# Optimization experiments

Hardware: AMD Instinct MI355X
Metric: run time of the kernel (lower is better)

Reference implementation:

```python
import jax, jax.numpy as jnp
import numpy as np

B, T, I, H = 512, 1024, 50, 32  # batch, seq_len, input_size, hidden_size


def setup_inputs() -> dict:
    key = jax.random.key(0)
    ks = jax.random.split(key, 13)
    s = 1.0 / np.sqrt(H)  # PyTorch LSTM/Linear uniform init bound

    def u(k, shape):
        return jax.random.uniform(k, shape, jnp.float32, -s, s)

    return {
        "x": jax.random.normal(ks[0], (B, T, I), jnp.float32),
        # forward direction LSTM params (gate order: i, f, g, o)
        "w_ih_f": u(ks[1], (4 * H, I)),
        "w_hh_f": u(ks[2], (4 * H, H)),
        "b_ih_f": u(ks[3], (4 * H,)),
        "b_hh_f": u(ks[4], (4 * H,)),
        # reverse direction LSTM params
        "w_ih_r": u(ks[5], (4 * H, I)),
        "w_hh_r": u(ks[6], (4 * H, H)),
        "b_ih_r": u(ks[7], (4 * H,)),
        "b_hh_r": u(ks[8], (4 * H,)),
        # FC head
        "fc1_w": u(ks[9], (2 * H, 2 * H)),
        "fc1_b": u(ks[10], (2 * H,)),
        "fc3_w": u(ks[11], (1, 2 * H)),
        "fc3_b": u(ks[12], (1,)),
    }


def _lstm_scan(x_proj, w_hh):
    # x_proj: (T, B, 4H) = precomputed input projections + biases
    b = x_proj.shape[1]
    h0 = jnp.zeros((b, H), x_proj.dtype)
    c0 = jnp.zeros((b, H), x_proj.dtype)

    def step(carry, xp):
        h, c = carry
        z = xp + h @ w_hh.T  # (B, 4H)
        i, f, g, o = jnp.split(z, 4, axis=-1)
        c = jax.nn.sigmoid(f) * c + jax.nn.sigmoid(i) * jnp.tanh(g)
        h = jax.nn.sigmoid(o) * jnp.tanh(c)
        return (h, c), h

    _, hs = jax.lax.scan(step, (h0, c0), x_proj)
    return hs  # (T, B, H)


def reference(x, w_ih_f, w_hh_f, b_ih_f, b_hh_f,
              w_ih_r, w_hh_r, b_ih_r, b_hh_r,
              fc1_w, fc1_b, fc3_w, fc3_b):
    xt = jnp.swapaxes(x, 0, 1)  # (T, B, I) time-major for scan
    # batch all input projections up front (big GEMM instead of per-step)
    pf = xt @ w_ih_f.T + (b_ih_f + b_hh_f)          # (T, B, 4H)
    pr = xt[::-1] @ w_ih_r.T + (b_ih_r + b_hh_r)    # reversed time

    hf = _lstm_scan(pf, w_hh_f)           # (T, B, H)
    hr = _lstm_scan(pr, w_hh_r)[::-1]     # flip back to forward time order

    out = jnp.concatenate([hf, hr], axis=-1)  # (T, B, 2H)
    out = jnp.swapaxes(out, 0, 1)             # (B, T, 2H)
    out = out @ fc1_w.T + fc1_b               # fc1
    # dropout(p=0.2) is identity in eval/inference mode
    out = out @ fc3_w.T + fc3_b               # fc3 -> (B, T, 1)
    return out
```

## Files before the change

### kernel.cpp

```cpp
#include <hip/hip_runtime.h>

#define BB 512
#define TT 1024
#define II 50
#define HH 32
#define CH 16
#define NCH (TT / CH)
#define RSLOT 32

typedef float v2f __attribute__((ext_vector_type(2)));
typedef float v4f __attribute__((ext_vector_type(4)));
typedef short v8s __attribute__((ext_vector_type(8)));

__device__ __forceinline__ float fast_rcp(float x) { return __builtin_amdgcn_rcpf(x); }
__device__ __forceinline__ float sigm(float x) { return fast_rcp(1.f + __expf(-x)); }
__device__ __forceinline__ float tanh_(float x) {
    return 1.f - 2.f * fast_rcp(1.f + __expf(2.f * x));
}
__device__ __forceinline__ float hadd(v2f v) { return v.x + v.y; }
__device__ __forceinline__ short bf16rne(float f) {
    unsigned u = __float_as_uint(f);
    u += 0x7FFF + ((u >> 16) & 1);
    return (short)(u >> 16);
}

__global__ void init_out_kernel(float* __restrict__ out,
                                const float* __restrict__ fc1_b,
                                const float* __restrict__ fc3_w,
                                const float* __restrict__ fc3_b,
                                int n) {
    int idx = blockIdx.x * blockDim.x + threadIdx.x;
    float b = fc3_b[0];
    #pragma unroll
    for (int k = 0; k < 64; ++k) b += fc3_w[k] * fc1_b[k];
    if (idx < n) out[idx] = b;
}

__global__ void __launch_bounds__(128, 1) lstm_pc_kernel(
    const float* __restrict__ x,
    const float* __restrict__ w_ih_f, const float* __restrict__ w_hh_f,
    const float* __restrict__ b_ih_f, const float* __restrict__ b_hh_f,
    const float* __restrict__ w_ih_r, const float* __restrict__ w_hh_r,
    const float* __restrict__ b_ih_r, const float* __restrict__ b_hh_r,
    const float* __restrict__ fc1_w, const float* __restrict__ fc3_w,
    float* __restrict__ out)
{
    __shared__ float ringF[RSLOT * 256];
    __shared__ float hbuf[2][HH][65];
    __shared__ __align__(16) float hst[64];

    const int tid  = threadIdx.x;
    const int lane = tid & 63;
    const int wave = tid >> 6;
    const int b    = blockIdx.x;
    float* outb = out + (size_t)b * TT;

    if (wave == 1) {
        const float* xb = x + (size_t)b * TT * II;
        const int nl = lane & 15;
        const int q  = lane >> 4;
        const float* wih[2] = {w_ih_f, w_ih_r};

        v8s Bf[2][8][2];
        #pragma unroll
        for (int d = 0; d < 2; ++d)
            #pragma unroll
            for (int nt = 0; nt < 8; ++nt) {
                const int n = nt * 16 + nl;
                #pragma unroll
                for (int kf = 0; kf < 2; ++kf)
                    #pragma unroll
                    for (int j = 0; j < 8; ++j) {
                        const int k = kf * 32 + q * 8 + j;
                        Bf[d][nt][kf][j] = (k < II) ? bf16rne(wih[d][n * II + k])
                                                    : (short)0;
                    }
            }

        auto cidx = [](int g) -> int {
            return (g < 32) ? 2 * g
                 : (g < 64) ? 2 * (g - 32) + 1
                 : (g < 96) ? 64 + 2 * (g - 64)
                            : 64 + 2 * (g - 96) + 1;
        };

        auto produce_chunk = [&](int c) {
            #pragma unroll
            for (int d = 0; d < 2; ++d) {
                const int S = c * CH + nl;
                const int t = d ? (TT - 1 - S) : S;
                const float* xr = xb + (size_t)t * II;
                v8s A0, A1;
                #pragma unroll
                for (int j = 0; j < 8; ++j) A0[j] = bf16rne(xr[q * 8 + j]);
                #pragma unroll
                for (int j = 0; j < 8; ++j) {
                    const int k = 32 + q * 8 + j;
                    A1[j] = (k < II) ? bf16rne(xr[k]) : (short)0;
                }
                #pragma unroll
                for (int nt = 0; nt < 8; ++nt) {
                    v4f acc = {0.f, 0.f, 0.f, 0.f};
                    acc = __builtin_amdgcn_mfma_f32_16x16x32_bf16(A0, Bf[d][nt][0], acc, 0, 0, 0);
                    acc = __builtin_amdgcn_mfma_f32_16x16x32_bf16(A1, Bf[d][nt][1], acc, 0, 0, 0);
                    const int col = d * 128 + cidx(nt * 16 + nl);
                    #pragma unroll
                    for (int r = 0; r < 4; ++r) {
                        const int slot = (c * CH + q * 4 + r) & (RSLOT - 1);
                        ringF[slot * 256 + col] = acc[r];
                    }
                }
            }
        };
        auto flush = [&](int m) {
            if (lane < 32) {
                const int d   = lane >> 4;
                const int idx = lane & 15;
                const int ti  = m * CH + idx;
                const int col = ti & 63;
                float d0 = 0.f, d1 = 0.f, d2 = 0.f, d3 = 0.f;
                #pragma unroll
                for (int k = 0; k < HH; k += 4) {
                    d0 += hbuf[d][k    ][col];
                    d1 += hbuf[d][k + 1][col];
                    d2 += hbuf[d][k + 2][col];
                    d3 += hbuf[d][k + 3][col];
                }
                const int t = d ? (TT - 1 - ti) : ti;
                atomicAdd(&outb[t], (d0 + d1) + (d2 + d3));
            }
        };

        produce_chunk(0);
        __syncthreads();
        for (int n = 0; n < NCH; ++n) {
            if (n + 1 < NCH) produce_chunk(n + 1);
            if (n >= 1) flush(n - 1);
            __syncthreads();
        }
        flush(NCH - 1);
    } else {
        const int d = lane >> 5;
        const int k = lane & 31;
        const float* w_hh = d ? w_hh_r : w_hh_f;
        const float* bi   = d ? b_ih_r : b_ih_f;
        const float* bh   = d ? b_hh_r : b_hh_f;

        v2f wp[4][16];
        float bb[4];
        #pragma unroll
        for (int D = 0; D < 4; ++D) {
            const int row = D * 32 + k;
            #pragma unroll
            for (int j = 0; j < 16; ++j) {
                wp[D][j].x = w_hh[row * HH + 2 * j];
                wp[D][j].y = w_hh[row * HH + 2 * j + 1];
            }
            bb[D] = bi[row] + bh[row];
        }

        float wc = 0.f;
        {
            const int j = d * HH + k;
            #pragma unroll
            for (int n = 0; n < 64; ++n) wc += fc3_w[n] * fc1_w[n * 64 + j];
        }

        hst[lane] = 0.f;
        float c = 0.f;

        __syncthreads();

        for (int n = 0; n < NCH; ++n) {
            const int slot0 = (n & 1) * CH;
            const int col0  = (n & 3) * CH;
            #pragma unroll
            for (int u = 0; u < CH; ++u) {
                const float* rp = &ringF[(slot0 + u) * 256 + d * 128 + 2 * k];
                const v2f xz1 = *(const v2f*)rp;
                const v2f xz2 = *(const v2f*)(rp + 64);

                float4 h4[8];
                #pragma unroll
                for (int j = 0; j < 8; ++j)
                    h4[j] = *(const float4*)&hst[d * 32 + 4 * j];

                v2f aA[4], aB[4];
                #pragma unroll
                for (int D = 0; D < 4; ++D) {
                    aA[D] = (v2f){bb[D], 0.f};
                    aB[D] = (v2f){0.f, 0.f};
                }
                #pragma unroll
                for (int j = 0; j < 8; ++j) {
                    v2f p0 = {h4[j].x, h4[j].y};
                    v2f p1 = {h4[j].z, h4[j].w};
                    #pragma unroll
                    for (int D = 0; D < 4; ++D) {
                        aA[D] = __builtin_elementwise_fma(p0, wp[D][2 * j    ], aA[D]);
                        aB[D] = __builtin_elementwise_fma(p1, wp[D][2 * j + 1], aB[D]);
                    }
                }
                const float zi = xz1.x + hadd(aA[0] + aB[0]);
                const float zf = xz1.y + hadd(aA[1] + aB[1]);
                const float zg = xz2.x + hadd(aA[2] + aB[2]);
                const float zo = xz2.y + hadd(aA[3] + aB[3]);

                const float gi = sigm(zi);
                const float gf = sigm(zf);
                const float gg = tanh_(zg);
                const float go = sigm(zo);

                c = fmaf(gf, c, gi * gg);
                const float h = go * tanh_(c);

                hst[lane] = h;
                hbuf[d][k][col0 + u] = h * wc;
                asm volatile("" ::: "memory");
            }
            __syncthreads();
        }
    }
}

extern "C" void kernel_launch(void* const* d_in, const int* in_sizes, int n_in,
                              void* d_out, int out_size, void* d_ws, size_t ws_size,
                              hipStream_t stream) {
    const float* x      = (const float*)d_in[0];
    const float* w_ih_f = (const float*)d_in[1];
    const float* w_hh_f = (const float*)d_in[2];
    const float* b_ih_f = (const float*)d_in[3];
    const float* b_hh_f = (const float*)d_in[4];
    const float* w_ih_r = (const float*)d_in[5];
    const float* w_hh_r = (const float*)d_in[6];
    const float* b_ih_r = (const float*)d_in[7];
    const float* b_hh_r = (const float*)d_in[8];
    const float* fc1_w  = (const float*)d_in[9];
    const float* fc1_b  = (const float*)d_in[10];
    const float* fc3_w  = (const float*)d_in[11];
    const float* fc3_b  = (const float*)d_in[12];
    float* out = (float*)d_out;

    const int n = BB * TT;
    init_out_kernel<<<(n + 255) / 256, 256, 0, stream>>>(out, fc1_b, fc3_w, fc3_b, n);

    lstm_pc_kernel<<<BB, 128, 0, stream>>>(
        x, w_ih_f, w_hh_f, b_ih_f, b_hh_f,
        w_ih_r, w_hh_r, b_ih_r, b_hh_r,
        fc1_w, fc3_w, out);
}
```

Before: 428.9 us.

## Use fp16 dot2 for recurrent matvec and prefetch chunk input projections

The recurrent h·W_hh product now stores the hidden state and weights as fp16 pairs and uses the v_dot2 f32-accumulate instruction. This halves the LDS reads of h per step and roughly halves the FMA instruction count on the serial critical path. The input projections for a whole chunk are also loaded into registers before the step loop. The cost is lower precision in h and W_hh, which may drift over 1024 recurrent steps, and higher register pressure.

```diff
diff --git a/kernel.cpp b/kernel.cpp
--- a/kernel.cpp
+++ b/kernel.cpp
@@ -11,18 +11,19 @@
 typedef float v2f __attribute__((ext_vector_type(2)));
 typedef float v4f __attribute__((ext_vector_type(4)));
 typedef short v8s __attribute__((ext_vector_type(8)));
+typedef _Float16 v2h __attribute__((ext_vector_type(2)));
 
 __device__ __forceinline__ float fast_rcp(float x) { return __builtin_amdgcn_rcpf(x); }
 __device__ __forceinline__ float sigm(float x) { return fast_rcp(1.f + __expf(-x)); }
 __device__ __forceinline__ float tanh_(float x) {
     return 1.f - 2.f * fast_rcp(1.f + __expf(2.f * x));
 }
-__device__ __forceinline__ float hadd(v2f v) { return v.x + v.y; }
 __device__ __forceinline__ short bf16rne(float f) {
     unsigned u = __float_as_uint(f);
     u += 0x7FFF + ((u >> 16) & 1);
     return (short)(u >> 16);
 }
+__device__ __forceinline__ v2h asv2h(int v) { return __builtin_bit_cast(v2h, v); }
 
 __global__ void init_out_kernel(float* __restrict__ out,
                                 const float* __restrict__ fc1_b,
@@ -47,7 +48,7 @@
 {
     __shared__ float ringF[RSLOT * 256];
     __shared__ float hbuf[2][HH][65];
-    __shared__ __align__(16) float hst[64];
+    __shared__ __align__(16) _Float16 hsth[64];
 
     const int tid  = threadIdx.x;
     const int lane = tid & 63;
@@ -146,15 +147,15 @@
         const float* bi   = d ? b_ih_r : b_ih_f;
         const float* bh   = d ? b_hh_r : b_hh_f;
 
-        v2f wp[4][16];
+        v2h wph[4][16];
         float bb[4];
         #pragma unroll
         for (int D = 0; D < 4; ++D) {
             const int row = D * 32 + k;
             #pragma unroll
             for (int j = 0; j < 16; ++j) {
-                wp[D][j].x = w_hh[row * HH + 2 * j];
-                wp[D][j].y = w_hh[row * HH + 2 * j + 1];
+                wph[D][j].x = (_Float16)w_hh[row * HH + 2 * j];
+                wph[D][j].y = (_Float16)w_hh[row * HH + 2 * j + 1];
             }
             bb[D] = bi[row] + bh[row];
         }
@@ -166,7 +167,7 @@
             for (int n = 0; n < 64; ++n) wc += fc3_w[n] * fc1_w[n * 64 + j];
         }
 
-        hst[lane] = 0.f;
+        hsth[lane] = (_Float16)0.f;
         float c = 0.f;
 
         __syncthreads();
@@ -174,37 +175,48 @@
         for (int n = 0; n < NCH; ++n) {
             const int slot0 = (n & 1) * CH;
             const int col0  = (n & 3) * CH;
+
+            v2f xz1b[CH], xz2b[CH];
             #pragma unroll
             for (int u = 0; u < CH; ++u) {
                 const float* rp = &ringF[(slot0 + u) * 256 + d * 128 + 2 * k];
-                const v2f xz1 = *(const v2f*)rp;
-                const v2f xz2 = *(const v2f*)(rp + 64);
-
-                float4 h4[8];
-                #pragma unroll
-                for (int j = 0; j < 8; ++j)
-                    h4[j] = *(const float4*)&hst[d * 32 + 4 * j];
-
-                v2f aA[4], aB[4];
+                xz1b[u] = *(const v2f*)rp;
+                xz2b[u] = *(const v2f*)(rp + 64);
+            }
+
+            #pragma unroll
+            for (int u = 0; u < CH; ++u) {
+                int4 hw0 = *(const int4*)&hsth[d * 32];
+                int4 hw1 = *(const int4*)&hsth[d * 32 + 8];
+                int4 hw2 = *(const int4*)&hsth[d * 32 + 16];
+                int4 hw3 = *(const int4*)&hsth[d * 32 + 24];
+
+                float zA[4], zB[4];
+                #pragma unroll
+                for (int D = 0; D < 4; ++D) { zA[D] = bb[D]; zB[D] = 0.f; }
                 #pragma unroll
                 for (int D = 0; D < 4; ++D) {
-                    aA[D] = (v2f){bb[D], 0.f};
-                    aB[D] = (v2f){0.f, 0.f};
-                }
-                #pragma unroll
-                for (int j = 0; j < 8; ++j) {
-                    v2f p0 = {h4[j].x, h4[j].y};
-                    v2f p1 = {h4[j].z, h4[j].w};
-                    #pragma unroll
-                    for (int D = 0; D < 4; ++D) {
-                        aA[D] = __builtin_elementwise_fma(p0, wp[D][2 * j    ], aA[D]);
-                        aB[D] = __builtin_elementwise_fma(p1, wp[D][2 * j + 1], aB[D]);
-                    }
-                }
-                const float zi = xz1.x + hadd(aA[0] + aB[0]);
-                const float zf = xz1.y + hadd(aA[1] + aB[1]);
-                const float zg = xz2.x + hadd(aA[2] + aB[2]);
-                const float zo = xz2.y + hadd(aA[3] + aB[3]);
+                    zA[D] = __builtin_amdgcn_fdot2(asv2h(hw0.x), wph[D][0],  zA[D], false);
+                    zB[D] = __builtin_amdgcn_fdot2(asv2h(hw0.y), wph[D][1],  zB[D], false);
+                    zA[D] = __builtin_amdgcn_fdot2(asv2h(hw0.z), wph[D][2],  zA[D], false);
+                    zB[D] = __builtin_amdgcn_fdot2(asv2h(hw0.w), wph[D][3],  zB[D], false);
+                    zA[D] = __builtin_amdgcn_fdot2(asv2h(hw1.x), wph[D][4],  zA[D], false);
+                    zB[D] = __builtin_amdgcn_fdot2(asv2h(hw1.y), wph[D][5],  zB[D], false);
+                    zA[D] = __builtin_amdgcn_fdot2(asv2h(hw1.z), wph[D][6],  zA[D], false);
+                    zB[D] = __builtin_amdgcn_fdot2(asv2h(hw1.w), wph[D][7],  zB[D], false);
+                    zA[D] = __builtin_amdgcn_fdot2(asv2h(hw2.x), wph[D][8],  zA[D], false);
+                    zB[D] = __builtin_amdgcn_fdot2(asv2h(hw2.y), wph[D][9],  zB[D], false);
+                    zA[D] = __builtin_amdgcn_fdot2(asv2h(hw2.z), wph[D][10], zA[D], false);
+                    zB[D] = __builtin_amdgcn_fdot2(asv2h(hw2.w), wph[D][11], zB[D], false);
+                    zA[D] = __builtin_amdgcn_fdot2(asv2h(hw3.x), wph[D][12], zA[D], false);
+                    zB[D] = __builtin_amdgcn_fdot2(asv2h(hw3.y), wph[D][13], zB[D], false);
+                    zA[D] = __builtin_amdgcn_fdot2(asv2h(hw3.z), wph[D][14], zA[D], false);
+                    zB[D] = __builtin_amdgcn_fdot2(asv2h(hw3.w), wph[D][15], zB[D], false);
+                }
+                const float zi = xz1b[u].x + (zA[0] + zB[0]);
+                const float zf = xz1b[u].y + (zA[1] + zB[1]);
+                const float zg = xz2b[u].x + (zA[2] + zB[2]);
+                const float zo = xz2b[u].y + (zA[3] + zB[3]);
 
                 const float gi = sigm(zi);
                 const float gf = sigm(zf);
@@ -214,7 +226,7 @@
                 c = fmaf(gf, c, gi * gg);
                 const float h = go * tanh_(c);
 
-                hst[lane] = h;
+                hsth[lane] = (_Float16)h;
                 hbuf[d][k][col0 + u] = h * wc;
                 asm volatile("" ::: "memory");
             }
```

Result: no change. 431.4 us (+0.6%).

## Process two batch rows per block with fp16 dot2 recurrence and fp16 ring

Applied to the files above, without the earlier changes.

Each block now handles two batch sequences, so the recurrent wave interleaves two independent LSTM chains to hide latency. The recurrent matvec switches from fp32 FMAs to packed fp16 fdot2 with fp16 weights and hidden state, and input projections are stored in LDS as fp16 to fit both sequences. Grid is halved to 256 blocks. This trades precision in h, W_hh and the projections for fewer instructions and better ILP on the serial critical path, but reduces the number of blocks available to fill the GPU.

```diff
diff --git a/kernel.cpp b/kernel.cpp
--- a/kernel.cpp
+++ b/kernel.cpp
@@ -11,18 +11,19 @@
 typedef float v2f __attribute__((ext_vector_type(2)));
 typedef float v4f __attribute__((ext_vector_type(4)));
 typedef short v8s __attribute__((ext_vector_type(8)));
+typedef _Float16 v2h __attribute__((ext_vector_type(2)));
 
 __device__ __forceinline__ float fast_rcp(float x) { return __builtin_amdgcn_rcpf(x); }
 __device__ __forceinline__ float sigm(float x) { return fast_rcp(1.f + __expf(-x)); }
 __device__ __forceinline__ float tanh_(float x) {
     return 1.f - 2.f * fast_rcp(1.f + __expf(2.f * x));
 }
-__device__ __forceinline__ float hadd(v2f v) { return v.x + v.y; }
 __device__ __forceinline__ short bf16rne(float f) {
     unsigned u = __float_as_uint(f);
     u += 0x7FFF + ((u >> 16) & 1);
     return (short)(u >> 16);
 }
+__device__ __forceinline__ v2h asv2h(int v) { return __builtin_bit_cast(v2h, v); }
 
 __global__ void init_out_kernel(float* __restrict__ out,
                                 const float* __restrict__ fc1_b,
@@ -45,18 +46,20 @@
     const float* __restrict__ fc1_w, const float* __restrict__ fc3_w,
     float* __restrict__ out)
 {
-    __shared__ float ringF[RSLOT * 256];
-    __shared__ float hbuf[2][HH][65];
-    __shared__ __align__(16) float hst[64];
+    __shared__ _Float16 ringH[RSLOT * 512];
+    __shared__ float hbuf[2][2][HH][33];
+    __shared__ __align__(16) _Float16 hsth[2][64];
 
     const int tid  = threadIdx.x;
     const int lane = tid & 63;
     const int wave = tid >> 6;
-    const int b    = blockIdx.x;
-    float* outb = out + (size_t)b * TT;
+    const int bp   = blockIdx.x;
+    const float* xb[2]  = {x + (size_t)(2 * bp) * TT * II,
+                           x + (size_t)(2 * bp + 1) * TT * II};
+    float* outp[2] = {out + (size_t)(2 * bp) * TT,
+                      out + (size_t)(2 * bp + 1) * TT};
 
     if (wave == 1) {
-        const float* xb = x + (size_t)b * TT * II;
         const int nl = lane & 15;
         const int q  = lane >> 4;
         const float* wih[2] = {w_ih_f, w_ih_r};
@@ -86,49 +89,50 @@
 
         auto produce_chunk = [&](int c) {
             #pragma unroll
-            for (int d = 0; d < 2; ++d) {
-                const int S = c * CH + nl;
-                const int t = d ? (TT - 1 - S) : S;
-                const float* xr = xb + (size_t)t * II;
-                v8s A0, A1;
+            for (int bb = 0; bb < 2; ++bb)
                 #pragma unroll
-                for (int j = 0; j < 8; ++j) A0[j] = bf16rne(xr[q * 8 + j]);
-                #pragma unroll
-                for (int j = 0; j < 8; ++j) {
-                    const int k = 32 + q * 8 + j;
-                    A1[j] = (k < II) ? bf16rne(xr[k]) : (short)0;
+                for (int d = 0; d < 2; ++d) {
+                    const int S = c * CH + nl;
+                    const int t = d ? (TT - 1 - S) : S;
+                    const float* xr = xb[bb] + (size_t)t * II;
+                    v8s A0, A1;
+                    #pragma unroll
+                    for (int j = 0; j < 8; ++j) A0[j] = bf16rne(xr[q * 8 + j]);
+                    #pragma unroll
+                    for (int j = 0; j < 8; ++j) {
+                        const int k = 32 + q * 8 + j;
+                        A1[j] = (k < II) ? bf16rne(xr[k]) : (short)0;
+                    }
+                    #pragma unroll
+                    for (int nt = 0; nt < 8; ++nt) {
+                        v4f acc = {0.f, 0.f, 0.f, 0.f};
+                        acc = __builtin_amdgcn_mfma_f32_16x16x32_bf16(A0, Bf[d][nt][0], acc, 0, 0, 0);
+                        acc = __builtin_amdgcn_mfma_f32_16x16x32_bf16(A1, Bf[d][nt][1], acc, 0, 0, 0);
+                        const int col = bb * 256 + d * 128 + cidx(nt * 16 + nl);
+                        #pragma unroll
+                        for (int r = 0; r < 4; ++r) {
+                            const int slot = (c * CH + q * 4 + r) & (RSLOT - 1);
+                            ringH[slot * 512 + col] = (_Float16)acc[r];
+                        }
+                    }
                 }
-                #pragma unroll
-                for (int nt = 0; nt < 8; ++nt) {
-                    v4f acc = {0.f, 0.f, 0.f, 0.f};
-                    acc = __builtin_amdgcn_mfma_f32_16x16x32_bf16(A0, Bf[d][nt][0], acc, 0, 0, 0);
-                    acc = __builtin_amdgcn_mfma_f32_16x16x32_bf16(A1, Bf[d][nt][1], acc, 0, 0, 0);
-                    const int col = d * 128 + cidx(nt * 16 + nl);
-                    #pragma unroll
-                    for (int r = 0; r < 4; ++r) {
-                        const int slot = (c * CH + q * 4 + r) & (RSLOT - 1);
-                        ringF[slot * 256 + col] = acc[r];
-                    }
-                }
-            }
         };
         auto flush = [&](int m) {
-            if (lane < 32) {
-                const int d   = lane >> 4;
-                const int idx = lane & 15;
-                const int ti  = m * CH + idx;
-                const int col = ti & 63;
-                float d0 = 0.f, d1 = 0.f, d2 = 0.f, d3 = 0.f;
-                #pragma unroll
-                for (int k = 0; k < HH; k += 4) {
-                    d0 += hbuf[d][k    ][col];
-                    d1 += hbuf[d][k + 1][col];
-                    d2 += hbuf[d][k + 2][col];
-                    d3 += hbuf[d][k + 3][col];
-                }
-                const int t = d ? (TT - 1 - ti) : ti;
-                atomicAdd(&outb[t], (d0 + d1) + (d2 + d3));
+            const int bb  = lane >> 5;
+            const int dd  = (lane >> 4) & 1;
+            const int idx = lane & 15;
+            const int ti  = m * CH + idx;
+            const int col = ti & 31;
+            float d0 = 0.f, d1 = 0.f, d2 = 0.f, d3 = 0.f;
+            #pragma unroll
+            for (int k = 0; k < HH; k += 4) {
+                d0 += hbuf[bb][dd][k    ][col];
+                d1 += hbuf[bb][dd][k + 1][col];
+                d2 += hbuf[bb][dd][k + 2][col];
+                d3 += hbuf[bb][dd][k + 3][col];
             }
+            const int t = dd ? (TT - 1 - ti) : ti;
+            atomicAdd(&outp[bb][t], (d0 + d1) + (d2 + d3));
         };
 
         produce_chunk(0);
@@ -146,17 +150,17 @@
         const float* bi   = d ? b_ih_r : b_ih_f;
         const float* bh   = d ? b_hh_r : b_hh_f;
 
-        v2f wp[4][16];
-        float bb[4];
+        v2h wph[4][16];
+        float bias4[4];
         #pragma unroll
         for (int D = 0; D < 4; ++D) {
             const int row = D * 32 + k;
             #pragma unroll
             for (int j = 0; j < 16; ++j) {
-                wp[D][j].x = w_hh[row * HH + 2 * j];
-                wp[D][j].y = w_hh[row * HH + 2 * j + 1];
+                wph[D][j].x = (_Float16)w_hh[row * HH + 2 * j];
+                wph[D][j].y = (_Float16)w_hh[row * HH + 2 * j + 1];
             }
-            bb[D] = bi[row] + bh[row];
+            bias4[D] = bi[row] + bh[row];
         }
 
         float wc = 0.f;
@@ -166,57 +170,106 @@
             for (int n = 0; n < 64; ++n) wc += fc3_w[n] * fc1_w[n * 64 + j];
         }
 
-        hst[lane] = 0.f;
-        float c = 0.f;
+        hsth[0][lane] = (_Float16)0.f;
+        hsth[1][lane] = (_Float16)0.f;
+        float cA = 0.f, cB = 0.f;
 
         __syncthreads();
 
         for (int n = 0; n < NCH; ++n) {
             const int slot0 = (n & 1) * CH;
-            const int col0  = (n & 3) * CH;
-            #pragma unroll
-            for (int u = 0; u < CH; ++u) {
-                const float* rp = &ringF[(slot0 + u) * 256 + d * 128 + 2 * k];
-                const v2f xz1 = *(const v2f*)rp;
-                const v2f xz2 = *(const v2f*)(rp + 64);
-
-                float4 h4[8];
+            const int col0  = (n & 1) * CH;
+            #pragma unroll
+            for (int half = 0; half < 2; ++half) {
+                int pA1[8], pA2[8], pB1[8], pB2[8];
                 #pragma unroll
-                for (int j = 0; j < 8; ++j)
-                    h4[j] = *(const float4*)&hst[d * 32 + 4 * j];
-
-                v2f aA[4], aB[4];
-                #pragma unroll
-                for (int D = 0; D < 4; ++D) {
-                    aA[D] = (v2f){bb[D], 0.f};
-                    aB[D] = (v2f){0.f, 0.f};
+                for (int u = 0; u < 8; ++u) {
+                    const int base = (slot0 + half * 8 + u) * 512 + d * 128 + 2 * k;
+                    pA1[u] = *(const int*)&ringH[base];
+                    pA2[u] = *(const int*)&ringH[base + 64];
+                    pB1[u] = *(const int*)&ringH[base + 256];
+                    pB2[u] = *(const int*)&ringH[base + 256 + 64];
                 }
                 #pragma unroll
-                for (int j = 0; j < 8; ++j) {
-                    v2f p0 = {h4[j].x, h4[j].y};
-                    v2f p1 = {h4[j].z, h4[j].w};
+                for (int u = 0; u < 8; ++u) {
+                    int4 aw0 = *(const int4*)&hsth[0][d * 32];
+                    int4 aw1 = *(const int4*)&hsth[0][d * 32 + 8];
+                    int4 aw2 = *(const int4*)&hsth[0][d * 32 + 16];
+                    int4 aw3 = *(const int4*)&hsth[0][d * 32 + 24];
+                    int4 bw0 = *(const int4*)&hsth[1][d * 32];
+                    int4 bw1 = *(const int4*)&hsth[1][d * 32 + 8];
+                    int4 bw2 = *(const int4*)&hsth[1][d * 32 + 16];
+                    int4 bw3 = *(const int4*)&hsth[1][d * 32 + 24];
+
+                    float zAa[4], zBa[4], zAb[4], zBb[4];
                     #pragma unroll
                     for (int D = 0; D < 4; ++D) {
-                        aA[D] = __builtin_elementwise_fma(p0, wp[D][2 * j    ], aA[D]);
-                        aB[D] = __builtin_elementwise_fma(p1, wp[D][2 * j + 1], aB[D]);
-                    }
+                        zAa[D] = bias4[D]; zBa[D] = 0.f;
+                        zAb[D] = bias4[D]; zBb[D] = 0.f;
+                    }
+                    #pragma unroll
+                    for (int D = 0; D < 4; ++D) {
+                        zAa[D] = __builtin_amdgcn_fdot2(asv2h(aw0.x), wph[D][0],  zAa[D], false);
+                        zAb[D] = __builtin_amdgcn_fdot2(asv2h(bw0.x), wph[D][0],  zAb[D], false);
+                        zBa[D] = __builtin_amdgcn_fdot2(asv2h(aw0.y), wph[D][1],  zBa[D], false);
+                        zBb[D] = __builtin_amdgcn_fdot2(asv2h(bw0.y), wph[D][1],  zBb[D], false);
+                        zAa[D] = __builtin_amdgcn_fdot2(asv2h(aw0.z), wph[D][2],  zAa[D], false);
+                        zAb[D] = __builtin_amdgcn_fdot2(asv2h(bw0.z), wph[D][2],  zAb[D], false);
+                        zBa[D] = __builtin_amdgcn_fdot2(asv2h(aw0.w), wph[D][3],  zBa[D], false);
+                        zBb[D] = __builtin_amdgcn_fdot2(asv2h(bw0.w), wph[D][3],  zBb[D], false);
+                        zAa[D] = __builtin_amdgcn_fdot2(asv2h(aw1.x), wph[D][4],  zAa[D], false);
+                        zAb[D] = __builtin_amdgcn_fdot2(asv2h(bw1.x), wph[D][4],  zAb[D], false);
+                        zBa[D] = __builtin_amdgcn_fdot2(asv2h(aw1.y), wph[D][5],  zBa[D], false);
+                        zBb[D] = __builtin_amdgcn_fdot2(asv2h(bw1.y), wph[D][5],  zBb[D], false);
+                        zAa[D] = __builtin_amdgcn_fdot2(asv2h(aw1.z), wph[D][6],  zAa[D], false);
+                        zAb[D] = __builtin_amdgcn_fdot2(asv2h(bw1.z), wph[D][6],  zAb[D], false);
+                        zBa[D] = __builtin_amdgcn_fdot2(asv2h(aw1.w), wph[D][7],  zBa[D], false);
+                        zBb[D] = __builtin_amdgcn_fdot2(asv2h(bw1.w), wph[D][7],  zBb[D], false);
+                        zAa[D] = __builtin_amdgcn_fdot2(asv2h(aw2.x), wph[D][8],  zAa[D], false);
+                        zAb[D] = __builtin_amdgcn_fdot2(asv2h(bw2.x), wph[D][8],  zAb[D], false);
+                        zBa[D] = __builtin_amdgcn_fdot2(asv2h(aw2.y), wph[D][9],  zBa[D], false);
+                        zBb[D] = __builtin_amdgcn_fdot2(asv2h(bw2.y), wph[D][9],  zBb[D], false);
+                        zAa[D] = __builtin_amdgcn_fdot2(asv2h(aw2.z), wph[D][10], zAa[D], false);
+                        zAb[D] = __builtin_amdgcn_fdot2(asv2h(bw2.z), wph[D][10], zAb[D], false);
+                        zBa[D] = __builtin_amdgcn_fdot2(asv2h(aw2.w), wph[D][11], zBa[D], false);
+                        zBb[D] = __builtin_amdgcn_fdot2(asv2h(bw2.w), wph[D][11], zBb[D], false);
+                        zAa[D] = __builtin_amdgcn_fdot2(asv2h(aw3.x), wph[D][12], zAa[D], false);
+                        zAb[D] = __builtin_amdgcn_fdot2(asv2h(bw3.x), wph[D][12], zAb[D], false);
+                        zBa[D] = __builtin_amdgcn_fdot2(asv2h(aw3.y), wph[D][13], zBa[D], false);
+                        zBb[D] = __builtin_amdgcn_fdot2(asv2h(bw3.y), wph[D][13], zBb[D], false);
+                        zAa[D] = __builtin_amdgcn_fdot2(asv2h(aw3.z), wph[D][14], zAa[D], false);
+                        zAb[D] = __builtin_amdgcn_fdot2(asv2h(bw3.z), wph[D][14], zAb[D], false);
+                        zBa[D] = __builtin_amdgcn_fdot2(asv2h(aw3.w), wph[D][15], zBa[D], false);
+                        zBb[D] = __builtin_amdgcn_fdot2(asv2h(bw3.w), wph[D][15], zBb[D], false);
+                    }
+                    const v2h pifA = asv2h(pA1[u]), pgoA = asv2h(pA2[u]);
+                    const v2h pifB = asv2h(pB1[u]), pgoB = asv2h(pB2[u]);
+                    const float ziA = (float)pifA.x + (zAa[0] + zBa[0]);
+                    const float zfA = (float)pifA.y + (zAa[1] + zBa[1]);
+                    const float zgA = (float)pgoA.x + (zAa[2] + zBa[2]);
+                    const float zoA = (float)pgoA.y + (zAa[3] + zBa[3]);
+                    const float ziB = (float)pifB.x + (zAb[0] + zBb[0]);
+                    const float zfB = (float)pifB.y + (zAb[1] + zBb[1]);
+                    const float zgB = (float)pgoB.x + (zAb[2] + zBb[2]);
+                    const float zoB = (float)pgoB.y + (zAb[3] + zBb[3]);
+
+                    const float giA = sigm(ziA), gfA = sigm(zfA);
+                    const float ggA = tanh_(zgA), goA = sigm(zoA);
+                    const float giB = sigm(ziB), gfB = sigm(zfB);
+                    const float ggB = tanh_(zgB), goB = sigm(zoB);
+
+                    cA = fmaf(gfA, cA, giA * ggA);
+                    cB = fmaf(gfB, cB, giB * ggB);
+                    const float hA = goA * tanh_(cA);
+                    const float hB = goB * tanh_(cB);
+
+                    hsth[0][lane] = (_Float16)hA;
+                    hsth[1][lane] = (_Float16)hB;
+                    const int col = col0 + half * 8 + u;
+                    hbuf[0][d][k][col] = hA * wc;
+                    hbuf[1][d][k][col] = hB * wc;
+                    asm volatile("" ::: "memory");
                 }
-                const float zi = xz1.x + hadd(aA[0] + aB[0]);
-                const float zf = xz1.y + hadd(aA[1] + aB[1]);
-                const float zg = xz2.x + hadd(aA[2] + aB[2]);
-                const float zo = xz2.y + hadd(aA[3] + aB[3]);
-
-                const float gi = sigm(zi);
-                const float gf = sigm(zf);
-                const float gg = tanh_(zg);
-                const float go = sigm(zo);
-
-                c = fmaf(gf, c, gi * gg);
-                const float h = go * tanh_(c);
-
-                hst[lane] = h;
-                hbuf[d][k][col0 + u] = h * wc;
-                asm volatile("" ::: "memory");
             }
             __syncthreads();
         }
@@ -244,7 +297,7 @@
     const int n = BB * TT;
     init_out_kernel<<<(n + 255) / 256, 256, 0, stream>>>(out, fc1_b, fc3_w, fc3_b, n);
 
-    lstm_pc_kernel<<<BB, 128, 0, stream>>>(
+    lstm_pc_kernel<<<BB / 2, 128, 0, stream>>>(
         x, w_ih_f, w_hh_f, b_ih_f, b_hh_f,
         w_ih_r, w_hh_r, b_ih_r, b_hh_r,
         fc1_w, fc3_w, out);
```

Measured after the change: 674.0 us. 57.1% more time.
